# Optimization experiments

Measured on AMD Instinct MI355X. Metric: run time of the kernel, lower is better.

## Reference

```python
import jax, jax.numpy as jnp
import numpy as np

GROUPS = 4
PPG = 16  # kv_channels // groups = 64 // 4
Q_CH = 256
KV_CH = 64


def setup_inputs() -> dict:
    key = jax.random.key(0)
    ks = jax.random.split(key, 7)
    N, T, L = 4, 64, 64
    q = jax.random.normal(ks[0], (N, L, L, Q_CH), dtype=jnp.float32)
    kv = jax.random.normal(ks[1], (N, T, L, L, KV_CH), dtype=jnp.float32)
    # torch nn.Linear weights, stored pre-transposed so y = x @ W
    s_q = 1.0 / np.sqrt(Q_CH)
    s_kv = 1.0 / np.sqrt(KV_CH)
    Wq = jax.random.uniform(ks[2], (Q_CH, KV_CH), jnp.float32, -s_q, s_q)
    Wk = jax.random.uniform(ks[3], (KV_CH, KV_CH), jnp.float32, -s_kv, s_kv)
    Wv = jax.random.uniform(ks[4], (KV_CH, KV_CH), jnp.float32, -s_kv, s_kv)
    Wout = jax.random.uniform(ks[5], (KV_CH, Q_CH), jnp.float32, -s_kv, s_kv)
    b_out = jax.random.uniform(ks[6], (Q_CH,), jnp.float32, -s_kv, s_kv)
    return {"q": q, "kv": kv, "Wq": Wq, "Wk": Wk, "Wv": Wv, "Wout": Wout, "b_out": b_out}


def reference(q, kv, Wq, Wk, Wv, Wout, b_out):
    N, L, _, _ = q.shape
    T = kv.shape[1]
    qh = (q @ Wq).reshape(N, L, L, GROUPS, PPG)                 # nijgc
    kh = (kv @ Wk).reshape(N, T, L, L, GROUPS, PPG)             # ntijgc
    vh = (kv @ Wv).reshape(N, T, L, L, GROUPS, PPG)             # ntijgc
    scale = 1.0 / jnp.sqrt(jnp.float32(PPG))
    attn = jnp.einsum('nijgc,ntijgc->ntijg', qh, kh) * scale    # scores over T per pixel
    attn = jax.nn.softmax(attn, axis=1)
    x = jnp.einsum('ntijg,ntijgc->nijgc', attn, vh).reshape(N, L, L, KV_CH)
    return x @ Wout + b_out
```

## Files before the change

### kernel.cpp

```cpp
#include <hip/hip_runtime.h>

typedef short short8 __attribute__((ext_vector_type(8)));
typedef short short4v __attribute__((ext_vector_type(4)));
typedef float f32x4 __attribute__((ext_vector_type(4)));

__device__ __forceinline__ float bf2f(unsigned short u) {
  union { unsigned int i; float f; } v; v.i = ((unsigned int)u) << 16; return v.f;
}
__device__ __forceinline__ unsigned short f2bf(float f) {
  unsigned int x = __float_as_uint(f);
  unsigned int r = (x + 0x7fffu + ((x >> 16) & 1u)) >> 16;
  return (unsigned short)r;
}

typedef __attribute__((address_space(1))) void* gas_t;
typedef __attribute__((address_space(3))) void* las_t;
__device__ __forceinline__ void async16(const float* g, float* l) {
  __builtin_amdgcn_global_load_lds((gas_t)g, (las_t)l, 16, 0, 0);
}

__global__ __launch_bounds__(256) void prep_kernel(
    const float* __restrict__ Wq, const float* __restrict__ Wk,
    const float* __restrict__ Wv, const float* __restrict__ Wout,
    unsigned short* __restrict__ Afrag, unsigned short* __restrict__ WVOfrag) {
  const int b = blockIdx.x, tid = threadIdx.x;
  if (b < 256) {
    const int p = b, g = tid >> 6, d = tid & 63;
    float s = 0.f;
#pragma unroll
    for (int c = 0; c < 16; ++c)
      s += Wq[p * 64 + g * 16 + c] * Wk[d * 64 + g * 16 + c];
    s *= 0.25f;
    const int n = g * 64 + d, k = p;
    Afrag[(size_t)(k >> 5) * 8192 + n * 32 + (k & 31)] = f2bf(s);
  } else {
    const int row = b - 256, g = row >> 6, d = row & 63, q = tid;
    float s = 0.f;
#pragma unroll
    for (int c = 0; c < 16; ++c)
      s += Wv[d * 64 + g * 16 + c] * Wout[(g * 16 + c) * 256 + q];
    WVOfrag[(size_t)(row >> 5) * 8192 + q * 32 + (row & 31)] = f2bf(s);
  }
}

template <int MODE>
__global__ __launch_bounds__(256) void gemm256_kernel(
    const void* __restrict__ Xv, const unsigned short* __restrict__ Wfrag,
    void* __restrict__ Outv, const float* __restrict__ bias) {
  __shared__ unsigned short A_s[32 * 40];
  const int tid = threadIdx.x;
  const int m0 = blockIdx.x * 32;
  const int w = tid >> 6, lane = tid & 63;
  const int m_l = lane & 15, quad = lane >> 4;
  const int nt0 = (w & 1) * 8, m16 = (w >> 1) * 16;
  const int srow = tid >> 3, sc4 = (tid & 7) * 4;

  f32x4 acc[8];
#pragma unroll
  for (int i = 0; i < 8; ++i) acc[i] = (f32x4){0.f, 0.f, 0.f, 0.f};

  for (int ks = 0; ks < 8; ++ks) {
    if (MODE == 0) {
      const float* X = (const float*)Xv;
      float4 x = *(const float4*)(X + (size_t)(m0 + srow) * 256 + ks * 32 + sc4);
      short4v vv;
      vv[0] = (short)f2bf(x.x); vv[1] = (short)f2bf(x.y);
      vv[2] = (short)f2bf(x.z); vv[3] = (short)f2bf(x.w);
      *(short4v*)&A_s[srow * 40 + sc4] = vv;
    } else {
      const unsigned short* X = (const unsigned short*)Xv;
      uint2 xv = *(const uint2*)(X + (size_t)(m0 + srow) * 256 + ks * 32 + sc4);
      *(uint2*)&A_s[srow * 40 + sc4] = xv;
    }
    __syncthreads();
    short8 a = *(const short8*)&A_s[(m16 + m_l) * 40 + quad * 8];
#pragma unroll
    for (int j = 0; j < 8; ++j) {
      const unsigned short* bp =
          Wfrag + ((size_t)ks * 256 + (nt0 + j) * 16 + m_l) * 32 + quad * 8;
      short8 bfr = *(const short8*)bp;
      acc[j] = __builtin_amdgcn_mfma_f32_16x16x32_bf16(a, bfr, acc[j], 0, 0, 0);
    }
    __syncthreads();
  }
  const int row0 = m0 + m16 + quad * 4;
#pragma unroll
  for (int j = 0; j < 8; ++j) {
    const int col = (nt0 + j) * 16 + m_l;
    if (MODE == 0) {
      unsigned short* Out = (unsigned short*)Outv;
#pragma unroll
      for (int r = 0; r < 4; ++r)
        Out[(size_t)(row0 + r) * 256 + col] = f2bf(acc[j][r]);
    } else {
      float* Out = (float*)Outv;
      const float bb = bias[col];
#pragma unroll
      for (int r = 0; r < 4; ++r)
        Out[(size_t)(row0 + r) * 256 + col] = acc[j][r] + bb;
    }
  }
}

__global__ __launch_bounds__(256, 1) void attn_kernel(
    const float* __restrict__ kv, const unsigned short* __restrict__ qk,
    unsigned short* __restrict__ yout) {
  __shared__ float kvbuf[3][4096];
  __shared__ unsigned short qk_s[16384];

  const int tid = threadIdx.x;
  const int wgid = blockIdx.x;
  const int n = wgid >> 6, i = wgid & 63;
  const int j = tid >> 2, g = tid & 3;
  const int w = tid >> 6, lane = tid & 63;

  const float* kvblk = kv + ((size_t)n << 24) + ((size_t)i << 12);
  const int loff = w * 1024 + lane * 4;

#pragma unroll
  for (int q = 0; q < 4; ++q)
    async16(kvblk + loff + q * 256, &kvbuf[0][loff + q * 256]);
#pragma unroll
  for (int q = 0; q < 4; ++q)
    async16(kvblk + (1 << 18) + loff + q * 256, &kvbuf[1][loff + q * 256]);

  const unsigned short* qkb = qk + ((size_t)wgid << 14);
#pragma unroll
  for (int it = 0; it < 8; ++it)
    *(uint4*)&qk_s[(it * 256 + tid) * 8] =
        *(const uint4*)(qkb + (it * 256 + tid) * 8);
  __syncthreads();

  float qf[64];
#pragma unroll
  for (int c = 0; c < 16; ++c) {
    const int rot = (c + j) & 15;
    uint2 u = *(const uint2*)&qk_s[j * 256 + g * 64 + rot * 4];
    qf[4 * c + 0] = bf2f((unsigned short)(u.x & 0xffffu));
    qf[4 * c + 1] = bf2f((unsigned short)(u.x >> 16));
    qf[4 * c + 2] = bf2f((unsigned short)(u.y & 0xffffu));
    qf[4 * c + 3] = bf2f((unsigned short)(u.y >> 16));
  }

  float yac[64];
#pragma unroll
  for (int c = 0; c < 64; ++c) yac[c] = 0.f;
  float lsum = 0.f;

  int b = 0, ib = 2;
  for (int t = 0; t < 64; ++t) {
    if (t >= 1) __syncthreads();
    if (t + 2 < 64) {
      const float* src = kvblk + ((size_t)(t + 2) << 18) + loff;
      float* dst = &kvbuf[ib][loff];
#pragma unroll
      for (int q = 0; q < 4; ++q) async16(src + q * 256, dst + q * 256);
    }
    const float* row = &kvbuf[b][j * 64];
    float s = 0.f;
    float4 cv[16];
#pragma unroll
    for (int c = 0; c < 16; ++c) {
      const int rot = (c + j) & 15;
      cv[c] = *(const float4*)(row + rot * 4);
      s = fmaf(cv[c].x, qf[4 * c + 0], s);
      s = fmaf(cv[c].y, qf[4 * c + 1], s);
      s = fmaf(cv[c].z, qf[4 * c + 2], s);
      s = fmaf(cv[c].w, qf[4 * c + 3], s);
    }
    const float p = __expf(s);
    lsum += p;
#pragma unroll
    for (int c = 0; c < 16; ++c) {
      yac[4 * c + 0] = fmaf(p, cv[c].x, yac[4 * c + 0]);
      yac[4 * c + 1] = fmaf(p, cv[c].y, yac[4 * c + 1]);
      yac[4 * c + 2] = fmaf(p, cv[c].z, yac[4 * c + 2]);
      yac[4 * c + 3] = fmaf(p, cv[c].w, yac[4 * c + 3]);
    }
    b = (b == 2) ? 0 : b + 1;
    ib = (ib == 2) ? 0 : ib + 1;
  }

  const float inv = 1.f / lsum;
  unsigned int* yst = (unsigned int*)qk_s;
#pragma unroll
  for (int c = 0; c < 16; ++c) {
    const int rot = (c + j) & 15;
    uint2 pk;
    pk.x = (unsigned int)f2bf(yac[4 * c + 0] * inv) |
           ((unsigned int)f2bf(yac[4 * c + 1] * inv) << 16);
    pk.y = (unsigned int)f2bf(yac[4 * c + 2] * inv) |
           ((unsigned int)f2bf(yac[4 * c + 3] * inv) << 16);
    *(uint2*)&yst[j * 128 + g * 32 + rot * 2] = pk;
  }
  __syncthreads();
  unsigned short* yo = yout + ((size_t)wgid << 14);
  const uint4* srcv = (const uint4*)qk_s;
#pragma unroll
  for (int it = 0; it < 8; ++it)
    *(uint4*)(yo + (it * 256 + tid) * 8) = srcv[it * 256 + tid];
}

extern "C" void kernel_launch(void* const* d_in, const int* in_sizes, int n_in,
                              void* d_out, int out_size, void* d_ws,
                              size_t ws_size, hipStream_t stream) {
  const float* q    = (const float*)d_in[0];
  const float* kv   = (const float*)d_in[1];
  const float* Wq   = (const float*)d_in[2];
  const float* Wk   = (const float*)d_in[3];
  const float* Wv   = (const float*)d_in[4];
  const float* Wout = (const float*)d_in[5];
  const float* bout = (const float*)d_in[6];

  unsigned short* ws      = (unsigned short*)d_ws;
  unsigned short* Afrag   = ws;
  unsigned short* WVOfrag = ws + 65536;
  unsigned short* qk_ws   = ws + 131072;
  unsigned short* y_ws    = ws + 131072 + 4194304;

  hipLaunchKernelGGL(prep_kernel, dim3(512), dim3(256), 0, stream,
                     Wq, Wk, Wv, Wout, Afrag, WVOfrag);
  hipLaunchKernelGGL((gemm256_kernel<0>), dim3(512), dim3(256), 0, stream,
                     (const void*)q, Afrag, (void*)qk_ws, (const float*)nullptr);
  hipLaunchKernelGGL(attn_kernel, dim3(256), dim3(256), 0, stream,
                     kv, qk_ws, y_ws);
  hipLaunchKernelGGL((gemm256_kernel<1>), dim3(512), dim3(256), 0, stream,
                     (const void*)y_ws, WVOfrag, d_out, bout);
}
```

Baseline: 436.0 us.

## Fuse q-projection GEMM, attention and output GEMM into one kernel

Measured after the change: 404.8 us. -7.2%, faster.

```diff
diff --git a/kernel.cpp b/kernel.cpp
--- a/kernel.cpp
+++ b/kernel.cpp
@@ -1,7 +1,6 @@
 #include <hip/hip_runtime.h>
 
 typedef short short8 __attribute__((ext_vector_type(8)));
-typedef short short4v __attribute__((ext_vector_type(4)));
 typedef float f32x4 __attribute__((ext_vector_type(4)));
 
 __device__ __forceinline__ float bf2f(unsigned short u) {
@@ -43,92 +42,65 @@
   }
 }
 
-template <int MODE>
-__global__ __launch_bounds__(256) void gemm256_kernel(
-    const void* __restrict__ Xv, const unsigned short* __restrict__ Wfrag,
-    void* __restrict__ Outv, const float* __restrict__ bias) {
-  __shared__ unsigned short A_s[32 * 40];
+__global__ __launch_bounds__(256, 1) void fused_kernel(
+    const float* __restrict__ q, const float* __restrict__ kv,
+    const unsigned short* __restrict__ Afrag,
+    const unsigned short* __restrict__ WVOfrag,
+    const float* __restrict__ bias, float* __restrict__ Out) {
+  __shared__ float kvbuf[3][4096];
+  __shared__ unsigned short qk_s[64 * 256];
+  __shared__ unsigned short A_s[64 * 40];
+
   const int tid = threadIdx.x;
-  const int m0 = blockIdx.x * 32;
+  const int wgid = blockIdx.x;
   const int w = tid >> 6, lane = tid & 63;
   const int m_l = lane & 15, quad = lane >> 4;
-  const int nt0 = (w & 1) * 8, m16 = (w >> 1) * 16;
-  const int srow = tid >> 3, sc4 = (tid & 7) * 4;
-
-  f32x4 acc[8];
-#pragma unroll
-  for (int i = 0; i < 8; ++i) acc[i] = (f32x4){0.f, 0.f, 0.f, 0.f};
-
-  for (int ks = 0; ks < 8; ++ks) {
-    if (MODE == 0) {
-      const float* X = (const float*)Xv;
-      float4 x = *(const float4*)(X + (size_t)(m0 + srow) * 256 + ks * 32 + sc4);
-      short4v vv;
-      vv[0] = (short)f2bf(x.x); vv[1] = (short)f2bf(x.y);
-      vv[2] = (short)f2bf(x.z); vv[3] = (short)f2bf(x.w);
-      *(short4v*)&A_s[srow * 40 + sc4] = vv;
-    } else {
-      const unsigned short* X = (const unsigned short*)Xv;
-      uint2 xv = *(const uint2*)(X + (size_t)(m0 + srow) * 256 + ks * 32 + sc4);
-      *(uint2*)&A_s[srow * 40 + sc4] = xv;
-    }
-    __syncthreads();
-    short8 a = *(const short8*)&A_s[(m16 + m_l) * 40 + quad * 8];
-#pragma unroll
-    for (int j = 0; j < 8; ++j) {
-      const unsigned short* bp =
-          Wfrag + ((size_t)ks * 256 + (nt0 + j) * 16 + m_l) * 32 + quad * 8;
-      short8 bfr = *(const short8*)bp;
-      acc[j] = __builtin_amdgcn_mfma_f32_16x16x32_bf16(a, bfr, acc[j], 0, 0, 0);
-    }
-    __syncthreads();
-  }
-  const int row0 = m0 + m16 + quad * 4;
-#pragma unroll
-  for (int j = 0; j < 8; ++j) {
-    const int col = (nt0 + j) * 16 + m_l;
-    if (MODE == 0) {
-      unsigned short* Out = (unsigned short*)Outv;
+  const int j = tid >> 2, g = tid & 3;
+
+  {
+    const float* qrow = q + (size_t)wgid * 64 * 256;
+    const int srow = tid >> 2, sc = (tid & 3) * 8;
+    f32x4 acc[16];
+#pragma unroll
+    for (int i = 0; i < 16; ++i) acc[i] = (f32x4){0.f, 0.f, 0.f, 0.f};
+    for (int ks = 0; ks < 8; ++ks) {
+      const float4* xp = (const float4*)(qrow + (size_t)srow * 256 + ks * 32 + sc);
+      float4 x0 = xp[0], x1 = xp[1];
+      short8 vv;
+      vv[0] = (short)f2bf(x0.x); vv[1] = (short)f2bf(x0.y);
+      vv[2] = (short)f2bf(x0.z); vv[3] = (short)f2bf(x0.w);
+      vv[4] = (short)f2bf(x1.x); vv[5] = (short)f2bf(x1.y);
+      vv[6] = (short)f2bf(x1.z); vv[7] = (short)f2bf(x1.w);
+      *(short8*)&A_s[srow * 40 + sc] = vv;
+      __syncthreads();
+      short8 a = *(const short8*)&A_s[(w * 16 + m_l) * 40 + quad * 8];
+#pragma unroll
+      for (int nt = 0; nt < 16; ++nt) {
+        short8 bf = *(const short8*)(Afrag +
+            ((size_t)ks * 256 + nt * 16 + m_l) * 32 + quad * 8);
+        acc[nt] = __builtin_amdgcn_mfma_f32_16x16x32_bf16(a, bf, acc[nt], 0, 0, 0);
+      }
+      __syncthreads();
+    }
+#pragma unroll
+    for (int nt = 0; nt < 16; ++nt) {
+      const int col = nt * 16 + m_l;
 #pragma unroll
       for (int r = 0; r < 4; ++r)
-        Out[(size_t)(row0 + r) * 256 + col] = f2bf(acc[j][r]);
-    } else {
-      float* Out = (float*)Outv;
-      const float bb = bias[col];
-#pragma unroll
-      for (int r = 0; r < 4; ++r)
-        Out[(size_t)(row0 + r) * 256 + col] = acc[j][r] + bb;
-    }
-  }
-}
-
-__global__ __launch_bounds__(256, 1) void attn_kernel(
-    const float* __restrict__ kv, const unsigned short* __restrict__ qk,
-    unsigned short* __restrict__ yout) {
-  __shared__ float kvbuf[3][4096];
-  __shared__ unsigned short qk_s[16384];
-
-  const int tid = threadIdx.x;
-  const int wgid = blockIdx.x;
-  const int n = wgid >> 6, i = wgid & 63;
-  const int j = tid >> 2, g = tid & 3;
-  const int w = tid >> 6, lane = tid & 63;
-
-  const float* kvblk = kv + ((size_t)n << 24) + ((size_t)i << 12);
+        qk_s[(w * 16 + quad * 4 + r) * 256 + col] = f2bf(acc[nt][r]);
+    }
+  }
+
+  const float* kvblk =
+      kv + ((size_t)(wgid >> 6) << 24) + ((size_t)(wgid & 63) << 12);
   const int loff = w * 1024 + lane * 4;
 
 #pragma unroll
-  for (int q = 0; q < 4; ++q)
-    async16(kvblk + loff + q * 256, &kvbuf[0][loff + q * 256]);
-#pragma unroll
-  for (int q = 0; q < 4; ++q)
-    async16(kvblk + (1 << 18) + loff + q * 256, &kvbuf[1][loff + q * 256]);
-
-  const unsigned short* qkb = qk + ((size_t)wgid << 14);
-#pragma unroll
-  for (int it = 0; it < 8; ++it)
-    *(uint4*)&qk_s[(it * 256 + tid) * 8] =
-        *(const uint4*)(qkb + (it * 256 + tid) * 8);
+  for (int qq = 0; qq < 4; ++qq)
+    async16(kvblk + loff + qq * 256, &kvbuf[0][loff + qq * 256]);
+#pragma unroll
+  for (int qq = 0; qq < 4; ++qq)
+    async16(kvblk + (1 << 18) + loff + qq * 256, &kvbuf[1][loff + qq * 256]);
   __syncthreads();
 
   float qf[64];
@@ -154,7 +126,7 @@
       const float* src = kvblk + ((size_t)(t + 2) << 18) + loff;
       float* dst = &kvbuf[ib][loff];
 #pragma unroll
-      for (int q = 0; q < 4; ++q) async16(src + q * 256, dst + q * 256);
+      for (int qq = 0; qq < 4; ++qq) async16(src + qq * 256, dst + qq * 256);
     }
     const float* row = &kvbuf[b][j * 64];
     float s = 0.f;
@@ -181,24 +153,45 @@
     ib = (ib == 2) ? 0 : ib + 1;
   }
 
-  const float inv = 1.f / lsum;
-  unsigned int* yst = (unsigned int*)qk_s;
-#pragma unroll
-  for (int c = 0; c < 16; ++c) {
-    const int rot = (c + j) & 15;
-    uint2 pk;
-    pk.x = (unsigned int)f2bf(yac[4 * c + 0] * inv) |
-           ((unsigned int)f2bf(yac[4 * c + 1] * inv) << 16);
-    pk.y = (unsigned int)f2bf(yac[4 * c + 2] * inv) |
-           ((unsigned int)f2bf(yac[4 * c + 3] * inv) << 16);
-    *(uint2*)&yst[j * 128 + g * 32 + rot * 2] = pk;
+  {
+    const float inv = 1.f / lsum;
+    unsigned int* yst = (unsigned int*)qk_s;
+#pragma unroll
+    for (int c = 0; c < 16; ++c) {
+      const int rot = (c + j) & 15;
+      uint2 pk;
+      pk.x = (unsigned int)f2bf(yac[4 * c + 0] * inv) |
+             ((unsigned int)f2bf(yac[4 * c + 1] * inv) << 16);
+      pk.y = (unsigned int)f2bf(yac[4 * c + 2] * inv) |
+             ((unsigned int)f2bf(yac[4 * c + 3] * inv) << 16);
+      *(uint2*)&yst[j * 128 + g * 32 + rot * 2] = pk;
+    }
   }
   __syncthreads();
-  unsigned short* yo = yout + ((size_t)wgid << 14);
-  const uint4* srcv = (const uint4*)qk_s;
-#pragma unroll
-  for (int it = 0; it < 8; ++it)
-    *(uint4*)(yo + (it * 256 + tid) * 8) = srcv[it * 256 + tid];
+
+  {
+    f32x4 acc[16];
+#pragma unroll
+    for (int i = 0; i < 16; ++i) acc[i] = (f32x4){0.f, 0.f, 0.f, 0.f};
+    for (int ks = 0; ks < 8; ++ks) {
+      short8 a = *(const short8*)&qk_s[(w * 16 + m_l) * 256 + ks * 32 + quad * 8];
+#pragma unroll
+      for (int nt = 0; nt < 16; ++nt) {
+        short8 bf = *(const short8*)(WVOfrag +
+            ((size_t)ks * 256 + nt * 16 + m_l) * 32 + quad * 8);
+        acc[nt] = __builtin_amdgcn_mfma_f32_16x16x32_bf16(a, bf, acc[nt], 0, 0, 0);
+      }
+    }
+    float* outb = Out + (size_t)wgid * 64 * 256;
+#pragma unroll
+    for (int nt = 0; nt < 16; ++nt) {
+      const int col = nt * 16 + m_l;
+      const float bb = bias[col];
+#pragma unroll
+      for (int r = 0; r < 4; ++r)
+        outb[(size_t)(w * 16 + quad * 4 + r) * 256 + col] = acc[nt][r] + bb;
+    }
+  }
 }
 
 extern "C" void kernel_launch(void* const* d_in, const int* in_sizes, int n_in,
@@ -215,15 +208,9 @@
   unsigned short* ws      = (unsigned short*)d_ws;
   unsigned short* Afrag   = ws;
   unsigned short* WVOfrag = ws + 65536;
-  unsigned short* qk_ws   = ws + 131072;
-  unsigned short* y_ws    = ws + 131072 + 4194304;
 
   hipLaunchKernelGGL(prep_kernel, dim3(512), dim3(256), 0, stream,
                      Wq, Wk, Wv, Wout, Afrag, WVOfrag);
-  hipLaunchKernelGGL((gemm256_kernel<0>), dim3(512), dim3(256), 0, stream,
-                     (const void*)q, Afrag, (void*)qk_ws, (const float*)nullptr);
-  hipLaunchKernelGGL(attn_kernel, dim3(256), dim3(256), 0, stream,
-                     kv, qk_ws, y_ws);
-  hipLaunchKernelGGL((gemm256_kernel<1>), dim3(512), dim3(256), 0, stream,
-                     (const void*)y_ws, WVOfrag, d_out, bout);
-}
+  hipLaunchKernelGGL(fused_kernel, dim3(256), dim3(256), 0, stream,
+                     q, kv, Afrag, WVOfrag, bout, (float*)d_out);
+}
```
